# Kernel tuning notes

Measured on AMD Instinct MI355X. Metric: run time of the kernel, lower is better.

Reference implementation:

```python
import jax, jax.numpy as jnp
import numpy as np


def _patch_size(w):
    # mirrors PatchLoss size selection (static shape -> Python branch is fine)
    if w == 512:
        return 64
    elif 256 <= w < 512:
        return 32
    raise ValueError('error size')


def setup_inputs() -> dict:
    key = jax.random.key(0)
    k1, k2 = jax.random.split(key)
    shape = (1, 3, 32, 512, 512)  # (b=1, c, t, h, w)
    x = jax.random.normal(k1, shape, dtype=jnp.float32)
    x_r = jax.random.normal(k2, shape, dtype=jnp.float32)
    return {"x": x, "x_r": x_r}


def reference(x, x_r):
    _, c, t, h, w = x.shape
    size = _patch_size(w)
    tc, hc, wc = 1, size // 2, size // 2
    # L = |(x+1)/2 - (x_r+1)/2| ; original detaches before pooling
    L = jnp.abs((x + 1.0) / 2.0 - (x_r + 1.0) / 2.0)
    D = jax.lax.stop_gradient(L)[0]  # (c, t, h, w), batch squeezed
    # patch means over (c, hc, wc) for each frame (tc=1) and spatial block
    nh, nw = h // hc, w // wc
    P = D.reshape(c, t, nh, hc, nw, wc).mean(axis=(0, 3, 5))  # (t, nh, nw)
    # max over spatial patches; original init max_patch=0.0, so clamp at 0
    max_patches = jnp.maximum(P.max(axis=(1, 2)), 0.0)  # (t,)
    return jnp.log(max_patches.mean())
```

## Files before the change

### kernel.cpp

```cpp
#include <hip/hip_runtime.h>
#include <math.h>
#include <stdint.h>


typedef float vf4 __attribute__((ext_vector_type(4)));
typedef __attribute__((address_space(1))) const void gas_void;
typedef __attribute__((address_space(3))) void lds_void;

__global__ __launch_bounds__(256) void patch_sum_kernel(
    const float* __restrict__ x, const float* __restrict__ xr,
    float* __restrict__ part) {
  __shared__ vf4 ldsA[1024];
  __shared__ vf4 ldsC[1024];
  const int b   = blockIdx.x;
  const int tid = threadIdx.x;
  const int wave = tid >> 6;
  const int lane = tid & 63;

  const vf4* a4 = (const vf4*)x  + (size_t)b * 1024;
  const vf4* c4 = (const vf4*)xr + (size_t)b * 1024;

#pragma unroll
  for (int i = 0; i < 4; ++i) {
    const int s = i * 4 + wave;
    __builtin_amdgcn_global_load_lds(
        (gas_void*)(uintptr_t)(a4 + (size_t)s * 64 + lane),
        (lds_void*)(uintptr_t)(ldsA + s * 64), 16, 0, 2 );
    __builtin_amdgcn_global_load_lds(
        (gas_void*)(uintptr_t)(c4 + (size_t)s * 64 + lane),
        (lds_void*)(uintptr_t)(ldsC + s * 64), 16, 0, 2 );
  }
  __builtin_amdgcn_s_waitcnt(0);
  __builtin_amdgcn_sched_barrier(0);

  float s0 = 0.f, s1 = 0.f, s2 = 0.f, s3 = 0.f;
#pragma unroll
  for (int i = 0; i < 4; ++i) {
    vf4 a = ldsA[i * 256 + tid];
    vf4 c = ldsC[i * 256 + tid];
    s0 += fabsf(a.x - c.x);
    s1 += fabsf(a.y - c.y);
    s2 += fabsf(a.z - c.z);
    s3 += fabsf(a.w - c.w);
  }
  float acc = (s0 + s1) + (s2 + s3);

  acc += __shfl_down(acc, 4, 8);
  acc += __shfl_down(acc, 2, 8);
  acc += __shfl_down(acc, 1, 8);
  __shared__ float sb[32];
  if ((tid & 7) == 0) sb[tid >> 3] = acc;
  __syncthreads();
  if (tid < 16) part[(size_t)b * 16 + tid] = sb[tid] + sb[tid + 16];
}

__global__ __launch_bounds__(1024) void finalize_kernel(
    const float* __restrict__ part, float* __restrict__ out) {
  const int tid = threadIdx.x;
  const int t = tid >> 5;
  const int j = tid & 31;
  float m = -1e30f;
#pragma unroll
  for (int k = 0; k < 8; ++k) {
    int p = t * 256 + j + 32 * k;
    int ph = (p >> 4) & 15;
    int pw = p & 15;
    float v = 0.f;
#pragma unroll
    for (int ch = 0; ch < 3; ++ch) {
#pragma unroll
      for (int q = 0; q < 4; ++q) {
        int idx = (ch * 2048 + t * 64 + ph * 4 + q) * 16 + pw;
        v += part[idx];
      }
    }
    m = fmaxf(m, v);
  }
#pragma unroll
  for (int o = 16; o > 0; o >>= 1) m = fmaxf(m, __shfl_down(m, o, 32));
  __shared__ float s[32];
  if (j == 0) s[t] = fmaxf(m * (0.5f / 3072.0f), 0.f);
  __syncthreads();
  if (tid < 32) {
    float v = s[tid];
#pragma unroll
    for (int o = 16; o > 0; o >>= 1) v += __shfl_down(v, o, 32);
    if (tid == 0) out[0] = logf(v * (1.0f / 32.0f));
  }
}

extern "C" void kernel_launch(void* const* d_in, const int* in_sizes, int n_in,
                              void* d_out, int out_size, void* d_ws, size_t ws_size,
                              hipStream_t stream) {
  const float* x  = (const float*)d_in[0];
  const float* xr = (const float*)d_in[1];
  float* part = (float*)d_ws;
  float* out  = (float*)d_out;

  patch_sum_kernel<<<6144, 256, 0, stream>>>(x, xr, part);
  finalize_kernel<<<1, 1024, 0, stream>>>(part, out);
}
```

Measured before the change: 196.5 us.

## Double per-block work, split loads between direct-to-LDS and register nontemporal loads

Each block now handles two 16KB chunks per input instead of one and the grid is halved. The second chunk is pulled into LDS with global_load_lds while the first is read straight into registers with nontemporal loads, so the two load paths overlap and more bytes are in flight per wave. The finalize kernel's indexing is adjusted to the new partial-sum layout, with two halves per patch row instead of four. Fewer blocks lowers launch and scheduling overhead, at the cost of more registers per thread and a smaller grid to spread across CUs.

```diff
diff --git a/kernel.cpp b/kernel.cpp
--- a/kernel.cpp
+++ b/kernel.cpp
@@ -12,36 +12,50 @@
     float* __restrict__ part) {
   __shared__ vf4 ldsA[1024];
   __shared__ vf4 ldsC[1024];
-  const int b   = blockIdx.x;
-  const int tid = threadIdx.x;
+  const int b    = blockIdx.x;
+  const int tid  = threadIdx.x;
   const int wave = tid >> 6;
   const int lane = tid & 63;
 
-  const vf4* a4 = (const vf4*)x  + (size_t)b * 1024;
-  const vf4* c4 = (const vf4*)xr + (size_t)b * 1024;
+  const vf4* a4 = (const vf4*)x  + (size_t)b * 2048;
+  const vf4* c4 = (const vf4*)xr + (size_t)b * 2048;
 
 #pragma unroll
   for (int i = 0; i < 4; ++i) {
     const int s = i * 4 + wave;
     __builtin_amdgcn_global_load_lds(
-        (gas_void*)(uintptr_t)(a4 + (size_t)s * 64 + lane),
+        (gas_void*)(uintptr_t)(a4 + 1024 + (size_t)s * 64 + lane),
         (lds_void*)(uintptr_t)(ldsA + s * 64), 16, 0, 2 );
     __builtin_amdgcn_global_load_lds(
-        (gas_void*)(uintptr_t)(c4 + (size_t)s * 64 + lane),
+        (gas_void*)(uintptr_t)(c4 + 1024 + (size_t)s * 64 + lane),
         (lds_void*)(uintptr_t)(ldsC + s * 64), 16, 0, 2 );
   }
-  __builtin_amdgcn_s_waitcnt(0);
-  __builtin_amdgcn_sched_barrier(0);
+
+  vf4 a[4], c[4];
+#pragma unroll
+  for (int i = 0; i < 4; ++i) a[i] = __builtin_nontemporal_load(&a4[i * 256 + tid]);
+#pragma unroll
+  for (int i = 0; i < 4; ++i) c[i] = __builtin_nontemporal_load(&c4[i * 256 + tid]);
 
   float s0 = 0.f, s1 = 0.f, s2 = 0.f, s3 = 0.f;
 #pragma unroll
   for (int i = 0; i < 4; ++i) {
-    vf4 a = ldsA[i * 256 + tid];
-    vf4 c = ldsC[i * 256 + tid];
-    s0 += fabsf(a.x - c.x);
-    s1 += fabsf(a.y - c.y);
-    s2 += fabsf(a.z - c.z);
-    s3 += fabsf(a.w - c.w);
+    s0 += fabsf(a[i].x - c[i].x);
+    s1 += fabsf(a[i].y - c[i].y);
+    s2 += fabsf(a[i].z - c[i].z);
+    s3 += fabsf(a[i].w - c[i].w);
+  }
+
+  __builtin_amdgcn_s_waitcnt(0);
+  __builtin_amdgcn_sched_barrier(0);
+#pragma unroll
+  for (int i = 0; i < 4; ++i) {
+    vf4 ah = ldsA[i * 256 + tid];
+    vf4 ch = ldsC[i * 256 + tid];
+    s0 += fabsf(ah.x - ch.x);
+    s1 += fabsf(ah.y - ch.y);
+    s2 += fabsf(ah.z - ch.z);
+    s3 += fabsf(ah.w - ch.w);
   }
   float acc = (s0 + s1) + (s2 + s3);
 
@@ -69,8 +83,8 @@
 #pragma unroll
     for (int ch = 0; ch < 3; ++ch) {
 #pragma unroll
-      for (int q = 0; q < 4; ++q) {
-        int idx = (ch * 2048 + t * 64 + ph * 4 + q) * 16 + pw;
+      for (int half = 0; half < 2; ++half) {
+        int idx = ((ch << 10) + (t << 5) + (ph << 1) + half) * 16 + pw;
         v += part[idx];
       }
     }
@@ -97,6 +111,6 @@
   float* part = (float*)d_ws;
   float* out  = (float*)d_out;
 
-  patch_sum_kernel<<<6144, 256, 0, stream>>>(x, xr, part);
+  patch_sum_kernel<<<3072, 256, 0, stream>>>(x, xr, part);
   finalize_kernel<<<1, 1024, 0, stream>>>(part, out);
 }
```

After: 194.5 us. About the same (-1.0%).
